# Kernel tuning notes

Measured on AMD Instinct MI355X. Metric: run time of the kernel, lower is better.

The kernel has to match this reference:

```python
import jax, jax.numpy as jnp
import numpy as np


def _ln(x, g, b, eps=1e-5):
    m = x.mean(-1, keepdims=True)
    v = ((x - m) ** 2).mean(-1, keepdims=True)
    return (x - m) * jax.lax.rsqrt(v + eps) * g + b


def setup_inputs() -> dict:
    key = jax.random.key(0)
    ks = jax.random.split(key, 16)
    B, C, D, H, W = 1, 192, 8, 32, 32
    nh, k, hid = 6, 7, 768
    n = lambda i, shape: jax.random.normal(ks[i], shape, dtype=jnp.float32) * 0.02
    return {
        'x': jax.random.normal(ks[0], (B, C, D, H, W), dtype=jnp.float32),
        'pos_emb': n(1, (1, D, C)),
        't_ln1_g': jnp.ones((C,), jnp.float32), 't_ln1_b': jnp.zeros((C,), jnp.float32),
        't_qkv_w': n(2, (C, 3 * C)),
        't_out_w': n(3, (C, C)), 't_out_b': jnp.zeros((C,), jnp.float32),
        't_ln2_g': jnp.ones((C,), jnp.float32), 't_ln2_b': jnp.zeros((C,), jnp.float32),
        't_fc1_w': n(4, (C, hid)), 't_fc1_b': jnp.zeros((hid,), jnp.float32),
        't_fc2_w': n(5, (hid, C)), 't_fc2_b': jnp.zeros((C,), jnp.float32),
        't_lnf_g': jnp.ones((C,), jnp.float32), 't_lnf_b': jnp.zeros((C,), jnp.float32),
        's_ln1_g': jnp.ones((C,), jnp.float32), 's_ln1_b': jnp.zeros((C,), jnp.float32),
        's_qkv_w': n(6, (C, 3 * C)), 's_qkv_b': jnp.zeros((3 * C,), jnp.float32),
        's_rpb': n(7, (nh, 2 * k - 1, 2 * k - 1)),
        's_proj_w': n(8, (C, C)), 's_proj_b': jnp.zeros((C,), jnp.float32),
        's_ln2_g': jnp.ones((C,), jnp.float32), 's_ln2_b': jnp.zeros((C,), jnp.float32),
        's_fc1_w': n(9, (C, hid)), 's_fc1_b': jnp.zeros((hid,), jnp.float32),
        's_fc2_w': n(10, (hid, C)), 's_fc2_b': jnp.zeros((C,), jnp.float32),
    }


def reference(x, pos_emb, t_ln1_g, t_ln1_b, t_qkv_w, t_out_w, t_out_b,
              t_ln2_g, t_ln2_b, t_fc1_w, t_fc1_b, t_fc2_w, t_fc2_b,
              t_lnf_g, t_lnf_b, s_ln1_g, s_ln1_b, s_qkv_w, s_qkv_b, s_rpb,
              s_proj_w, s_proj_b, s_ln2_g, s_ln2_b, s_fc1_w, s_fc1_b,
              s_fc2_w, s_fc2_b):
    B, C, D, H, W = x.shape
    nh = 6
    d = C // nh
    k = 7
    scale = d ** -0.5

    # ---- Time transformer: attend over the D frames per spatial position ----
    t = jnp.transpose(x, (0, 3, 4, 2, 1)).reshape(B * H * W, D, C)  # (b h w) s c
    t = t + pos_emb
    y = _ln(t, t_ln1_g, t_ln1_b)
    qkv = (y @ t_qkv_w).reshape(-1, D, 3, nh, d)
    q, kk, v = [jnp.transpose(qkv[:, :, i], (0, 2, 1, 3)) for i in range(3)]  # [N,nh,D,d]
    att = jax.nn.softmax(jnp.einsum('nhid,nhjd->nhij', q, kk) * scale, axis=-1)
    o = jnp.einsum('nhij,nhjd->nhid', att, v)
    o = jnp.transpose(o, (0, 2, 1, 3)).reshape(-1, D, C)
    t = t + (o @ t_out_w + t_out_b)
    y = _ln(t, t_ln2_g, t_ln2_b)
    t = t + (jax.nn.gelu(y @ t_fc1_w + t_fc1_b, approximate=False) @ t_fc2_w + t_fc2_b)
    t = _ln(t, t_lnf_g, t_lnf_b)
    x = x + jnp.transpose(t.reshape(B, H, W, D, C), (0, 4, 3, 1, 2))

    # ---- Space transformer: neighborhood (NAT) attention per frame ----
    s = jnp.transpose(x, (0, 2, 3, 4, 1)).reshape(B * D, H, W, C)  # (b s) h w c
    shortcut = s
    y = _ln(s, s_ln1_g, s_ln1_b)
    qkv = (y @ s_qkv_w + s_qkv_b).reshape(B * D, H, W, 3, nh, d)
    qkv = jnp.transpose(qkv, (3, 0, 4, 1, 2, 5))  # [3,N,nh,H,W,d]
    q, kk, v = qkv[0] * scale, qkv[1], qkv[2]
    half = k // 2
    sh = jnp.clip(jnp.arange(H) - half, 0, H - k)   # window start per row (edge-clamped)
    sw = jnp.clip(jnp.arange(W) - half, 0, W - k)
    idx_h = sh[:, None] + jnp.arange(k)             # [H,k] neighbor rows
    idx_w = sw[:, None] + jnp.arange(k)             # [W,k] neighbor cols
    rel_h = idx_h - jnp.arange(H)[:, None] + (k - 1)  # rel-pos-bias indices in [0,2k-2]
    rel_w = idx_w - jnp.arange(W)[:, None] + (k - 1)
    Kn = kk[:, :, idx_h][:, :, :, :, idx_w]  # [N,nh,H,k,W,k,d]
    Vn = v[:, :, idx_h][:, :, :, :, idx_w]
    att = jnp.einsum('nehwd,nehawbd->nehwab', q, Kn)  # [N,nh,H,W,k,k]
    bias = jnp.transpose(s_rpb[:, rel_h][:, :, :, rel_w], (0, 1, 3, 2, 4))  # [nh,H,W,k,k]
    att = att + bias[None]
    shp = att.shape
    att = jax.nn.softmax(att.reshape(shp[0], shp[1], shp[2], shp[3], k * k), axis=-1).reshape(shp)
    o = jnp.einsum('nehwab,nehawbd->nehwd', att, Vn)
    o = jnp.transpose(o, (0, 2, 3, 1, 4)).reshape(B * D, H, W, C)
    s = shortcut + (o @ s_proj_w + s_proj_b)
    y = _ln(s, s_ln2_g, s_ln2_b)
    s = s + (jax.nn.gelu(y @ s_fc1_w + s_fc1_b, approximate=False) @ s_fc2_w + s_fc2_b)
    x_space = jnp.transpose(s.reshape(B, D, H, W, C), (0, 4, 1, 2, 3))
    return x + x_space
```

## Files before the change

kernel.cpp:

```cpp
#include <hip/hip_runtime.h>
#include <hip/hip_bf16.h>
#include <math.h>

typedef __hip_bfloat16 bf16;
typedef short bf16x8 __attribute__((ext_vector_type(8)));
typedef float f32x4 __attribute__((ext_vector_type(4)));

__device__ __forceinline__ float b2f(bf16 v) { return __bfloat162float(v); }
__device__ __forceinline__ bf16 f2b(float v) { return __float2bfloat16(v); }
__device__ __forceinline__ float us2f(unsigned short u) {
  return __uint_as_float(((unsigned)u) << 16);
}
__device__ __forceinline__ unsigned short f2us(float f) {
  bf16 h = __float2bfloat16(f);
  return *reinterpret_cast<unsigned short*>(&h);
}
__device__ __forceinline__ float ldin(const void* p, size_t i, int f32) {
  return f32 ? ((const float*)p)[i] : b2f(((const bf16*)p)[i]);
}

#define CC 192
#define DD 8
#define HH 32
#define WW 32
#define NHEAD 6
#define HDIM 32
#define HID 768
#define NTOK 8192
#define ATT_SCALE 0.17677669529663687f

__global__ void probe_dtype_kernel(const unsigned short* __restrict__ xu,
                                   int* __restrict__ flag) {
  if (threadIdx.x == 0 && blockIdx.x == 0) {
    int insane = 0;
    for (int i = 0; i < 256; i++) {
      float v = us2f(xu[i]);
      float a = fabsf(v);
      bool sane = (a == 0.0f) || (a > 9.5e-7f && a < 64.0f);
      if (!sane) insane++;
    }
    *flag = (insane > 32) ? 1 : 0;
  }
}

__global__ void build_ln1_kernel(const void* __restrict__ x, const void* __restrict__ pos,
                                 const void* __restrict__ g, const void* __restrict__ b,
                                 float* __restrict__ T, bf16* __restrict__ Y,
                                 const int* __restrict__ dfl) {
  int f32 = *dfl;
  int wave = (blockIdx.x * blockDim.x + threadIdx.x) >> 6;
  int lane = threadIdx.x & 63;
  if (wave >= NTOK) return;
  int d = wave & 7, hw = wave >> 3;
  float v[3];
#pragma unroll
  for (int e = 0; e < 3; e++) {
    int c = lane + e * 64;
    v[e] = ldin(x, (size_t)((c << 3) + d) * 1024 + hw, f32) +
           ldin(pos, (size_t)d * CC + c, f32);
  }
  float* tr = T + (size_t)wave * CC;
#pragma unroll
  for (int e = 0; e < 3; e++) tr[lane + e * 64] = v[e];
  float s = v[0] + v[1] + v[2];
  for (int off = 32; off; off >>= 1) s += __shfl_xor(s, off);
  float mean = s * (1.0f / CC);
  float d0 = v[0] - mean, d1 = v[1] - mean, d2 = v[2] - mean;
  float q = d0 * d0 + d1 * d1 + d2 * d2;
  for (int off = 32; off; off >>= 1) q += __shfl_xor(q, off);
  float rstd = rsqrtf(q * (1.0f / CC) + 1e-5f);
  bf16* o = Y + (size_t)wave * CC;
  o[lane]       = f2b(d0 * rstd * ldin(g, lane, f32)       + ldin(b, lane, f32));
  o[lane + 64]  = f2b(d1 * rstd * ldin(g, lane + 64, f32)  + ldin(b, lane + 64, f32));
  o[lane + 128] = f2b(d2 * rstd * ldin(g, lane + 128, f32) + ldin(b, lane + 128, f32));
}

__global__ void ln_kernel(const float* __restrict__ in, bf16* __restrict__ out,
                          const void* __restrict__ g, const void* __restrict__ b,
                          int rows, const int* __restrict__ dfl) {
  int f32 = *dfl;
  int wave = (blockIdx.x * blockDim.x + threadIdx.x) >> 6;
  int lane = threadIdx.x & 63;
  if (wave >= rows) return;
  const float* r = in + (size_t)wave * CC;
  float v0 = r[lane], v1 = r[lane + 64], v2 = r[lane + 128];
  float s = v0 + v1 + v2;
  for (int off = 32; off; off >>= 1) s += __shfl_xor(s, off);
  float mean = s * (1.0f / CC);
  float d0 = v0 - mean, d1 = v1 - mean, d2 = v2 - mean;
  float q = d0 * d0 + d1 * d1 + d2 * d2;
  for (int off = 32; off; off >>= 1) q += __shfl_xor(q, off);
  float rstd = rsqrtf(q * (1.0f / CC) + 1e-5f);
  bf16* o = out + (size_t)wave * CC;
  o[lane]       = f2b(d0 * rstd * ldin(g, lane, f32)       + ldin(b, lane, f32));
  o[lane + 64]  = f2b(d1 * rstd * ldin(g, lane + 64, f32)  + ldin(b, lane + 64, f32));
  o[lane + 128] = f2b(d2 * rstd * ldin(g, lane + 128, f32) + ldin(b, lane + 128, f32));
}

template <int TM, bool BIAS, bool GELU, bool RES, bool OUTBF, bool FINAL>
__global__ void gemm_kernel(const bf16* __restrict__ A, const void* __restrict__ W,
                            const void* __restrict__ bias, const float* __restrict__ R,
                            void* __restrict__ Cout, const float* __restrict__ X2,
                            int M, int N, int K, const int* __restrict__ dfl) {
  int f32 = *dfl;
  __shared__ __align__(16) unsigned short As[TM * 64 * 40];
  __shared__ __align__(16) unsigned short Bs[64 * 40];
  int bm = blockIdx.y * (TM * 64), bn = blockIdx.x * 64;
  int tid = threadIdx.x;
  int w = tid >> 6;
  int lane = tid & 63;
  int lm = lane & 15;
  int lk = lane >> 4;

  f32x4 acc[TM][4];
#pragma unroll
  for (int i = 0; i < TM; i++)
#pragma unroll
    for (int j = 0; j < 4; j++) acc[i][j] = (f32x4){0.f, 0.f, 0.f, 0.f};

  const unsigned short* Au = reinterpret_cast<const unsigned short*>(A);

  for (int k0 = 0; k0 < K; k0 += 32) {
#pragma unroll
    for (int u = 0; u < TM; u++) {
      int unit = tid + u * 256;
      int row = unit >> 2, seg = unit & 3;
      uint4 v = *reinterpret_cast<const uint4*>(
          &Au[(size_t)(bm + row) * K + k0 + seg * 8]);
      *reinterpret_cast<uint4*>(&As[row * 40 + seg * 8]) = v;
    }
    {
      int e0 = tid * 8;
      int kk = e0 >> 6, n0 = e0 & 63;
      unsigned short vals[8];
      if (f32) {
        const float* Wf = (const float*)W + (size_t)(k0 + kk) * N + bn + n0;
        float4 w0 = *reinterpret_cast<const float4*>(Wf);
        float4 w1 = *reinterpret_cast<const float4*>(Wf + 4);
        vals[0] = f2us(w0.x); vals[1] = f2us(w0.y); vals[2] = f2us(w0.z); vals[3] = f2us(w0.w);
        vals[4] = f2us(w1.x); vals[5] = f2us(w1.y); vals[6] = f2us(w1.z); vals[7] = f2us(w1.w);
      } else {
        const unsigned short* Wb = (const unsigned short*)W + (size_t)(k0 + kk) * N + bn + n0;
        ushort4 u0 = *reinterpret_cast<const ushort4*>(Wb);
        ushort4 u1 = *reinterpret_cast<const ushort4*>(Wb + 4);
        vals[0] = u0.x; vals[1] = u0.y; vals[2] = u0.z; vals[3] = u0.w;
        vals[4] = u1.x; vals[5] = u1.y; vals[6] = u1.z; vals[7] = u1.w;
      }
#pragma unroll
      for (int j = 0; j < 8; j++) Bs[(n0 + j) * 40 + kk] = vals[j];
    }
    __syncthreads();

    bf16x8 af[TM], bfr[4];
#pragma unroll
    for (int tm = 0; tm < TM; tm++)
      af[tm] = *reinterpret_cast<const bf16x8*>(
          &As[(w * (TM * 16) + tm * 16 + lm) * 40 + lk * 8]);
#pragma unroll
    for (int tn = 0; tn < 4; tn++)
      bfr[tn] = *reinterpret_cast<const bf16x8*>(
          &Bs[(tn * 16 + lm) * 40 + lk * 8]);
#pragma unroll
    for (int tm = 0; tm < TM; tm++)
#pragma unroll
      for (int tn = 0; tn < 4; tn++)
        acc[tm][tn] = __builtin_amdgcn_mfma_f32_16x16x32_bf16(
            af[tm], bfr[tn], acc[tm][tn], 0, 0, 0);
    __syncthreads();
  }

#pragma unroll
  for (int tn = 0; tn < 4; tn++) {
    int col = bn + tn * 16 + lm;
    float bv = BIAS ? ldin(bias, col, f32) : 0.f;
#pragma unroll
    for (int tm = 0; tm < TM; tm++) {
      int row0 = bm + w * (TM * 16) + tm * 16 + lk * 4;
#pragma unroll
      for (int r = 0; r < 4; r++) {
        int row = row0 + r;
        float v = acc[tm][tn][r];
        if (BIAS) v += bv;
        if (GELU) v = 0.5f * v * (1.0f + erff(v * 0.70710678118654752f));
        size_t idx = (size_t)row * N + col;
        if (RES) v += R[idx];
        if (FINAL) {
          float o = v + X2[(size_t)row * CC + col];
          if (f32) ((float*)Cout)[(size_t)col * NTOK + row] = o;
          else     ((bf16*)Cout)[(size_t)col * NTOK + row] = f2b(o);
        } else if (OUTBF) {
          ((bf16*)Cout)[idx] = f2b(v);
        } else {
          ((float*)Cout)[idx] = v;
        }
      }
    }
  }
}

__global__ void time_attn_kernel(const bf16* __restrict__ qkv, bf16* __restrict__ O) {
  __shared__ float q[NHEAD][DD][HDIM];
  __shared__ float k[NHEAD][DD][HDIM];
  __shared__ float v[NHEAD][DD][HDIM];
  __shared__ float p[NHEAD][DD][DD];
  int n = blockIdx.x;
  int head = threadIdx.x >> 5;
  int dd = threadIdx.x & 31;
  for (int s = 0; s < DD; s++) {
    const bf16* row = qkv + (size_t)(n * DD + s) * (3 * CC);
    q[head][s][dd] = b2f(row[head * HDIM + dd]);
    k[head][s][dd] = b2f(row[CC + head * HDIM + dd]);
    v[head][s][dd] = b2f(row[2 * CC + head * HDIM + dd]);
  }
  __syncthreads();
  for (int pair = dd; pair < 64; pair += 32) {
    int sq = pair >> 3, sk = pair & 7;
    float sum = 0.f;
#pragma unroll
    for (int e = 0; e < HDIM; e++) sum += q[head][sq][e] * k[head][sk][e];
    p[head][sq][sk] = sum * ATT_SCALE;
  }
  __syncthreads();
  if (dd < DD) {
    float mx = -1e30f;
    for (int sk = 0; sk < DD; sk++) mx = fmaxf(mx, p[head][dd][sk]);
    float sum = 0.f;
    for (int sk = 0; sk < DD; sk++) { float e = expf(p[head][dd][sk] - mx); p[head][dd][sk] = e; sum += e; }
    float inv = 1.0f / sum;
    for (int sk = 0; sk < DD; sk++) p[head][dd][sk] *= inv;
  }
  __syncthreads();
  for (int sq = 0; sq < DD; sq++) {
    float sum = 0.f;
#pragma unroll
    for (int sk = 0; sk < DD; sk++) sum += p[head][sq][sk] * v[head][sk][dd];
    O[(size_t)(n * DD + sq) * CC + head * HDIM + dd] = f2b(sum);
  }
}

__global__ void epi_ln1_kernel(const float* __restrict__ T, const void* __restrict__ x,
                               const void* __restrict__ gf, const void* __restrict__ bf,
                               const void* __restrict__ g1, const void* __restrict__ b1,
                               float* __restrict__ X1T, bf16* __restrict__ Y,
                               const int* __restrict__ dfl) {
  int f32 = *dfl;
  int wave = (blockIdx.x * blockDim.x + threadIdx.x) >> 6;
  int lane = threadIdx.x & 63;
  if (wave >= NTOK) return;
  const float* r = T + (size_t)wave * CC;
  float v0 = r[lane], v1 = r[lane + 64], v2 = r[lane + 128];
  float s = v0 + v1 + v2;
  for (int off = 32; off; off >>= 1) s += __shfl_xor(s, off);
  float mean = s * (1.0f / CC);
  float d0 = v0 - mean, d1 = v1 - mean, d2 = v2 - mean;
  float q = d0 * d0 + d1 * d1 + d2 * d2;
  for (int off = 32; off; off >>= 1) q += __shfl_xor(q, off);
  float rstd = rsqrtf(q * (1.0f / CC) + 1e-5f);
  int d = wave & 7, hw = wave >> 3;
  int m = d * 1024 + hw;
  float xv[3];
#pragma unroll
  for (int e = 0; e < 3; e++) {
    int c = lane + e * 64;
    float dv = (e == 0 ? d0 : (e == 1 ? d1 : d2));
    float normed = dv * rstd * ldin(gf, c, f32) + ldin(bf, c, f32);
    xv[e] = ldin(x, (size_t)((c << 3) + d) * 1024 + hw, f32) + normed;
  }
  float* o = X1T + (size_t)m * CC;
#pragma unroll
  for (int e = 0; e < 3; e++) o[lane + e * 64] = xv[e];
  float s2 = xv[0] + xv[1] + xv[2];
  for (int off = 32; off; off >>= 1) s2 += __shfl_xor(s2, off);
  float mean2 = s2 * (1.0f / CC);
  float e0 = xv[0] - mean2, e1 = xv[1] - mean2, e2 = xv[2] - mean2;
  float q2 = e0 * e0 + e1 * e1 + e2 * e2;
  for (int off = 32; off; off >>= 1) q2 += __shfl_xor(q2, off);
  float rstd2 = rsqrtf(q2 * (1.0f / CC) + 1e-5f);
  bf16* y = Y + (size_t)m * CC;
  y[lane]       = f2b(e0 * rstd2 * ldin(g1, lane, f32)       + ldin(b1, lane, f32));
  y[lane + 64]  = f2b(e1 * rstd2 * ldin(g1, lane + 64, f32)  + ldin(b1, lane + 64, f32));
  y[lane + 128] = f2b(e2 * rstd2 * ldin(g1, lane + 128, f32) + ldin(b1, lane + 128, f32));
}

#define NKEY 224
#define PKS 40
#define PVS 232
__global__ void nat_attn_kernel(const bf16* __restrict__ qkv, const void* __restrict__ rpb,
                                bf16* __restrict__ O, const int* __restrict__ dfl) {
  int f32 = *dfl;
  __shared__ __align__(16) unsigned short Ks[NKEY * PKS];
  __shared__ __align__(16) unsigned short Vs[32 * PVS];
  __shared__ __align__(16) unsigned short Qs[64 * PKS];
  __shared__ __align__(16) unsigned short Ps[64 * PVS];
  __shared__ float rb[176];

  int blk = blockIdx.x;
  int frame = blk & 7;
  int rest = blk >> 3;
  int h = rest % 6;
  int tile = rest / 6;
  int ty = tile >> 2, tx = tile & 3;
  int base_h = min(max(ty * 8 - 3, 0), HH - 7);
  int base_w = min(max(tx * 8 - 3, 0), WW - 7);

  int tid = threadIdx.x;

  for (int i = tid; i < 169; i += 256) rb[i] = ldin(rpb, (size_t)h * 169 + i, f32);
  for (int u = tid; u < 784; u += 256) {
    int j = u >> 2, seg = u & 3;
    int a = j / 14, bb = j - a * 14;
    int ih = min(base_h + a, HH - 1), iw = min(base_w + bb, WW - 1);
    int mg = frame * 1024 + ih * 32 + iw;
    uint4 v = *reinterpret_cast<const uint4*>(qkv + (size_t)mg * 576 + 192 + h * 32 + seg * 8);
    *reinterpret_cast<uint4*>(&Ks[j * PKS + seg * 8]) = v;
  }
  for (int u = tid; u < 784; u += 256) {
    int j = u >> 2, seg = u & 3;
    int a = j / 14, bb = j - a * 14;
    int ih = min(base_h + a, HH - 1), iw = min(base_w + bb, WW - 1);
    int mg = frame * 1024 + ih * 32 + iw;
    uint4 v = *reinterpret_cast<const uint4*>(qkv + (size_t)mg * 576 + 384 + h * 32 + seg * 8);
    unsigned arr[4] = {v.x, v.y, v.z, v.w};
#pragma unroll
    for (int e = 0; e < 4; e++) {
      Vs[(seg * 8 + e * 2) * PVS + j]     = (unsigned short)(arr[e] & 0xffffu);
      Vs[(seg * 8 + e * 2 + 1) * PVS + j] = (unsigned short)(arr[e] >> 16);
    }
  }
  for (int u = tid; u < 32 * (PVS - 196); u += 256) {
    int dd = u / (PVS - 196), c = 196 + u % (PVS - 196);
    Vs[dd * PVS + c] = 0;
  }
  {
    int q = tid >> 2, seg = tid & 3;
    int qy = ty * 8 + (q >> 3), qx = tx * 8 + (q & 7);
    int mg = frame * 1024 + qy * 32 + qx;
    uint4 v = *reinterpret_cast<const uint4*>(qkv + (size_t)mg * 576 + h * 32 + seg * 8);
    *reinterpret_cast<uint4*>(&Qs[q * PKS + seg * 8]) = v;
  }
  __syncthreads();

  int w = tid >> 6;
  int lane = tid & 63;
  int c = lane & 15;
  int lk = lane >> 4;

  bf16x8 aq = *reinterpret_cast<const bf16x8*>(&Qs[(w * 16 + c) * PKS + lk * 8]);
  f32x4 sc[14];
#pragma unroll
  for (int f = 0; f < 14; f++) {
    bf16x8 bk = *reinterpret_cast<const bf16x8*>(&Ks[(f * 16 + c) * PKS + lk * 8]);
    sc[f] = __builtin_amdgcn_mfma_f32_16x16x32_bf16(aq, bk, (f32x4){0.f, 0.f, 0.f, 0.f}, 0, 0, 0);
  }

#pragma unroll
  for (int f = 0; f < 14; f++) {
    int key = f * 16 + c;
    int a = key / 14, bb = key - a * 14;
    int ih = base_h + a, iw = base_w + bb;
    bool keyok = key < 196;
#pragma unroll
    for (int r = 0; r < 4; r++) {
      int qloc = w * 16 + lk * 4 + r;
      int qy = ty * 8 + (qloc >> 3), qx = tx * 8 + (qloc & 7);
      int sh = min(max(qy - 3, 0), HH - 7);
      int sw = min(max(qx - 3, 0), WW - 7);
      bool valid = keyok && ((unsigned)(ih - sh) < 7u) && ((unsigned)(iw - sw) < 7u);
      int bidx = valid ? (ih - qy + 6) * 13 + (iw - qx + 6) : 0;
      float s = sc[f][r] * ATT_SCALE + rb[bidx];
      sc[f][r] = valid ? s : -1e30f;
    }
  }

  float mx[4], sm[4];
#pragma unroll
  for (int r = 0; r < 4; r++) {
    float m = sc[0][r];
#pragma unroll
    for (int f = 1; f < 14; f++) m = fmaxf(m, sc[f][r]);
    for (int off = 8; off; off >>= 1) m = fmaxf(m, __shfl_xor(m, off));
    mx[r] = m;
    float s = 0.f;
#pragma unroll
    for (int f = 0; f < 14; f++) { float e = __expf(sc[f][r] - m); sc[f][r] = e; s += e; }
    for (int off = 8; off; off >>= 1) s += __shfl_xor(s, off);
    sm[r] = 1.0f / s;
  }
#pragma unroll
  for (int f = 0; f < 14; f++)
#pragma unroll
    for (int r = 0; r < 4; r++)
      Ps[(w * 16 + lk * 4 + r) * PVS + f * 16 + c] = f2us(sc[f][r] * sm[r]);
  __syncthreads();

  f32x4 oacc[2] = {(f32x4){0.f, 0.f, 0.f, 0.f}, (f32x4){0.f, 0.f, 0.f, 0.f}};
#pragma unroll
  for (int kt = 0; kt < 7; kt++) {
    bf16x8 ap = *reinterpret_cast<const bf16x8*>(&Ps[(w * 16 + c) * PVS + kt * 32 + lk * 8]);
#pragma unroll
    for (int dt = 0; dt < 2; dt++) {
      bf16x8 bv = *reinterpret_cast<const bf16x8*>(&Vs[(dt * 16 + c) * PVS + kt * 32 + lk * 8]);
      oacc[dt] = __builtin_amdgcn_mfma_f32_16x16x32_bf16(ap, bv, oacc[dt], 0, 0, 0);
    }
  }

#pragma unroll
  for (int dt = 0; dt < 2; dt++)
#pragma unroll
    for (int r = 0; r < 4; r++) {
      int qloc = w * 16 + lk * 4 + r;
      int qy = ty * 8 + (qloc >> 3), qx = tx * 8 + (qloc & 7);
      int mg = frame * 1024 + qy * 32 + qx;
      O[(size_t)mg * CC + h * 32 + dt * 16 + c] = f2b(oacc[dt][r]);
    }
}

extern "C" void kernel_launch(void* const* d_in, const int* in_sizes, int n_in,
                              void* d_out, int out_size, void* d_ws, size_t ws_size,
                              hipStream_t stream) {
  const void* x        = d_in[0];
  const void* pos_emb  = d_in[1];
  const void* t_ln1_g  = d_in[2];
  const void* t_ln1_b  = d_in[3];
  const void* t_qkv_w  = d_in[4];
  const void* t_out_w  = d_in[5];
  const void* t_out_b  = d_in[6];
  const void* t_ln2_g  = d_in[7];
  const void* t_ln2_b  = d_in[8];
  const void* t_fc1_w  = d_in[9];
  const void* t_fc1_b  = d_in[10];
  const void* t_fc2_w  = d_in[11];
  const void* t_fc2_b  = d_in[12];
  const void* t_lnf_g  = d_in[13];
  const void* t_lnf_b  = d_in[14];
  const void* s_ln1_g  = d_in[15];
  const void* s_ln1_b  = d_in[16];
  const void* s_qkv_w  = d_in[17];
  const void* s_qkv_b  = d_in[18];
  const void* s_rpb    = d_in[19];
  const void* s_proj_w = d_in[20];
  const void* s_proj_b = d_in[21];
  const void* s_ln2_g  = d_in[22];
  const void* s_ln2_b  = d_in[23];
  const void* s_fc1_w  = d_in[24];
  const void* s_fc1_b  = d_in[25];
  const void* s_fc2_w  = d_in[26];
  const void* s_fc2_b  = d_in[27];

  float* ws = (float*)d_ws;
  const size_t SZ = (size_t)NTOK * CC;
  const size_t need = (5 * SZ + 4) * sizeof(float);
  if (ws_size < need) return;

  float* T   = ws;
  float* X1T = ws + SZ;
  bf16*  Y   = (bf16*)(ws + 2 * SZ);
  bf16*  O   = (bf16*)(ws + 2 * SZ + SZ / 2);
  bf16*  QKV = (bf16*)(ws + 3 * SZ);
  bf16*  Hb  = QKV;
  float* S   = T;
  int*   dfl = (int*)(ws + 5 * SZ);

  dim3 blk256(256);

  probe_dtype_kernel<<<1, 64, 0, stream>>>((const unsigned short*)x, dfl);

  build_ln1_kernel<<<NTOK / 4, blk256, 0, stream>>>(x, pos_emb, t_ln1_g, t_ln1_b, T, Y, dfl);
  gemm_kernel<2, false, false, false, true, false><<<dim3(9, 64), blk256, 0, stream>>>(
      Y, t_qkv_w, nullptr, nullptr, QKV, nullptr, NTOK, 3 * CC, CC, dfl);
  time_attn_kernel<<<1024, 192, 0, stream>>>(QKV, O);
  gemm_kernel<1, true, false, true, false, false><<<dim3(3, 128), blk256, 0, stream>>>(
      O, t_out_w, t_out_b, T, T, nullptr, NTOK, CC, CC, dfl);
  ln_kernel<<<NTOK / 4, blk256, 0, stream>>>(T, Y, t_ln2_g, t_ln2_b, NTOK, dfl);
  gemm_kernel<2, true, true, false, true, false><<<dim3(12, 64), blk256, 0, stream>>>(
      Y, t_fc1_w, t_fc1_b, nullptr, Hb, nullptr, NTOK, HID, CC, dfl);
  gemm_kernel<1, true, false, true, false, false><<<dim3(3, 128), blk256, 0, stream>>>(
      Hb, t_fc2_w, t_fc2_b, T, T, nullptr, NTOK, CC, HID, dfl);
  epi_ln1_kernel<<<NTOK / 4, blk256, 0, stream>>>(
      T, x, t_lnf_g, t_lnf_b, s_ln1_g, s_ln1_b, X1T, Y, dfl);

  gemm_kernel<2, true, false, false, true, false><<<dim3(9, 64), blk256, 0, stream>>>(
      Y, s_qkv_w, s_qkv_b, nullptr, QKV, nullptr, NTOK, 3 * CC, CC, dfl);
  nat_attn_kernel<<<768, blk256, 0, stream>>>(QKV, s_rpb, O, dfl);
  gemm_kernel<1, true, false, true, false, false><<<dim3(3, 128), blk256, 0, stream>>>(
      O, s_proj_w, s_proj_b, X1T, S, nullptr, NTOK, CC, CC, dfl);
  ln_kernel<<<NTOK / 4, blk256, 0, stream>>>(S, Y, s_ln2_g, s_ln2_b, NTOK, dfl);
  gemm_kernel<2, true, true, false, true, false><<<dim3(12, 64), blk256, 0, stream>>>(
      Y, s_fc1_w, s_fc1_b, nullptr, Hb, nullptr, NTOK, HID, CC, dfl);
  gemm_kernel<1, true, false, true, false, true><<<dim3(3, 128), blk256, 0, stream>>>(
      Hb, s_fc2_w, s_fc2_b, S, d_out, X1T, NTOK, CC, HID, dfl);
}
```

Measured before the change: 304.6 us.

## Pre-transpose weights to bf16 and widen GEMM K-tile to 64

Adds a kernel that converts all eight weight matrices once per call into transposed bf16 [N,K] layout in workspace. The GEMM then loads B tiles with 16-byte vector copies instead of per-element scattered shared-memory stores and fp32-to-bf16 conversion. The K tile is doubled to 64 with padded LDS rows, halving the number of barriers per GEMM. It also parallelizes the dtype probe across a wave. The cost is one extra launch that moves about 5 MB of weights, plus more shared memory per block.

```diff
diff --git a/kernel.cpp b/kernel.cpp
--- a/kernel.cpp
+++ b/kernel.cpp
@@ -31,17 +31,45 @@
 
 __global__ void probe_dtype_kernel(const unsigned short* __restrict__ xu,
                                    int* __restrict__ flag) {
-  if (threadIdx.x == 0 && blockIdx.x == 0) {
-    int insane = 0;
-    for (int i = 0; i < 256; i++) {
-      float v = us2f(xu[i]);
-      float a = fabsf(v);
-      bool sane = (a == 0.0f) || (a > 9.5e-7f && a < 64.0f);
-      if (!sane) insane++;
-    }
-    *flag = (insane > 32) ? 1 : 0;
-  }
-}
+  int lane = threadIdx.x;
+  int insane = 0;
+  for (int i = lane; i < 256; i += 64) {
+    float a = fabsf(us2f(xu[i]));
+    bool sane = (a == 0.0f) || (a > 9.5e-7f && a < 64.0f);
+    if (!sane) insane++;
+  }
+  for (int off = 32; off; off >>= 1) insane += __shfl_xor(insane, off);
+  if (lane == 0) *flag = (insane > 32) ? 1 : 0;
+}
+
+__global__ void wconv_kernel(const void* w0, const void* w1, const void* w2,
+                             const void* w3, const void* w4, const void* w5,
+                             const void* w6, const void* w7,
+                             bf16* __restrict__ WT, const int* __restrict__ dfl) {
+  int f32 = *dfl;
+  int idx = blockIdx.x * 256 + threadIdx.x;
+  if (idx >= 884736) return;
+  const void* src; int K, N, loc;
+  if      (idx < 110592) { src = w0; K = 192; N = 576; loc = idx; }
+  else if (idx < 147456) { src = w1; K = 192; N = 192; loc = idx - 110592; }
+  else if (idx < 294912) { src = w2; K = 192; N = 768; loc = idx - 147456; }
+  else if (idx < 442368) { src = w3; K = 768; N = 192; loc = idx - 294912; }
+  else if (idx < 552960) { src = w4; K = 192; N = 576; loc = idx - 442368; }
+  else if (idx < 589824) { src = w5; K = 192; N = 192; loc = idx - 552960; }
+  else if (idx < 737280) { src = w6; K = 192; N = 768; loc = idx - 589824; }
+  else                   { src = w7; K = 768; N = 192; loc = idx - 737280; }
+  int n = loc / K, k = loc - n * K;
+  WT[idx] = f2b(ldin(src, (size_t)k * N + n, f32));
+}
+
+#define WOFF_TQKV  0
+#define WOFF_TOUT  110592
+#define WOFF_TFC1  147456
+#define WOFF_TFC2  294912
+#define WOFF_SQKV  442368
+#define WOFF_SPROJ 552960
+#define WOFF_SFC1  589824
+#define WOFF_SFC2  737280
 
 __global__ void build_ln1_kernel(const void* __restrict__ x, const void* __restrict__ pos,
                                  const void* __restrict__ g, const void* __restrict__ b,
@@ -98,13 +126,13 @@
 }
 
 template <int TM, bool BIAS, bool GELU, bool RES, bool OUTBF, bool FINAL>
-__global__ void gemm_kernel(const bf16* __restrict__ A, const void* __restrict__ W,
+__global__ void gemm_kernel(const bf16* __restrict__ A, const bf16* __restrict__ WT,
                             const void* __restrict__ bias, const float* __restrict__ R,
                             void* __restrict__ Cout, const float* __restrict__ X2,
                             int M, int N, int K, const int* __restrict__ dfl) {
   int f32 = *dfl;
-  __shared__ __align__(16) unsigned short As[TM * 64 * 40];
-  __shared__ __align__(16) unsigned short Bs[64 * 40];
+  __shared__ __align__(16) unsigned short As[TM * 64 * 72];
+  __shared__ __align__(16) unsigned short Bs[64 * 72];
   int bm = blockIdx.y * (TM * 64), bn = blockIdx.x * 64;
   int tid = threadIdx.x;
   int w = tid >> 6;
@@ -119,53 +147,45 @@
     for (int j = 0; j < 4; j++) acc[i][j] = (f32x4){0.f, 0.f, 0.f, 0.f};
 
   const unsigned short* Au = reinterpret_cast<const unsigned short*>(A);
-
-  for (int k0 = 0; k0 < K; k0 += 32) {
-#pragma unroll
-    for (int u = 0; u < TM; u++) {
+  const unsigned short* Wu = reinterpret_cast<const unsigned short*>(WT);
+
+  for (int k0 = 0; k0 < K; k0 += 64) {
+#pragma unroll
+    for (int u = 0; u < TM * 2; u++) {
       int unit = tid + u * 256;
-      int row = unit >> 2, seg = unit & 3;
+      int row = unit >> 3, seg = unit & 7;
       uint4 v = *reinterpret_cast<const uint4*>(
           &Au[(size_t)(bm + row) * K + k0 + seg * 8]);
-      *reinterpret_cast<uint4*>(&As[row * 40 + seg * 8]) = v;
-    }
-    {
-      int e0 = tid * 8;
-      int kk = e0 >> 6, n0 = e0 & 63;
-      unsigned short vals[8];
-      if (f32) {
-        const float* Wf = (const float*)W + (size_t)(k0 + kk) * N + bn + n0;
-        float4 w0 = *reinterpret_cast<const float4*>(Wf);
-        float4 w1 = *reinterpret_cast<const float4*>(Wf + 4);
-        vals[0] = f2us(w0.x); vals[1] = f2us(w0.y); vals[2] = f2us(w0.z); vals[3] = f2us(w0.w);
-        vals[4] = f2us(w1.x); vals[5] = f2us(w1.y); vals[6] = f2us(w1.z); vals[7] = f2us(w1.w);
-      } else {
-        const unsigned short* Wb = (const unsigned short*)W + (size_t)(k0 + kk) * N + bn + n0;
-        ushort4 u0 = *reinterpret_cast<const ushort4*>(Wb);
-        ushort4 u1 = *reinterpret_cast<const ushort4*>(Wb + 4);
-        vals[0] = u0.x; vals[1] = u0.y; vals[2] = u0.z; vals[3] = u0.w;
-        vals[4] = u1.x; vals[5] = u1.y; vals[6] = u1.z; vals[7] = u1.w;
-      }
-#pragma unroll
-      for (int j = 0; j < 8; j++) Bs[(n0 + j) * 40 + kk] = vals[j];
+      *reinterpret_cast<uint4*>(&As[row * 72 + seg * 8]) = v;
+    }
+#pragma unroll
+    for (int u = 0; u < 2; u++) {
+      int unit = tid + u * 256;
+      int n = unit >> 3, seg = unit & 7;
+      uint4 v = *reinterpret_cast<const uint4*>(
+          &Wu[(size_t)(bn + n) * K + k0 + seg * 8]);
+      *reinterpret_cast<uint4*>(&Bs[n * 72 + seg * 8]) = v;
     }
     __syncthreads();
 
-    bf16x8 af[TM], bfr[4];
-#pragma unroll
-    for (int tm = 0; tm < TM; tm++)
-      af[tm] = *reinterpret_cast<const bf16x8*>(
-          &As[(w * (TM * 16) + tm * 16 + lm) * 40 + lk * 8]);
-#pragma unroll
-    for (int tn = 0; tn < 4; tn++)
-      bfr[tn] = *reinterpret_cast<const bf16x8*>(
-          &Bs[(tn * 16 + lm) * 40 + lk * 8]);
-#pragma unroll
-    for (int tm = 0; tm < TM; tm++)
+#pragma unroll
+    for (int kc = 0; kc < 2; kc++) {
+      bf16x8 af[TM], bfr[4];
+#pragma unroll
+      for (int tm = 0; tm < TM; tm++)
+        af[tm] = *reinterpret_cast<const bf16x8*>(
+            &As[(w * (TM * 16) + tm * 16 + lm) * 72 + kc * 32 + lk * 8]);
 #pragma unroll
       for (int tn = 0; tn < 4; tn++)
-        acc[tm][tn] = __builtin_amdgcn_mfma_f32_16x16x32_bf16(
-            af[tm], bfr[tn], acc[tm][tn], 0, 0, 0);
+        bfr[tn] = *reinterpret_cast<const bf16x8*>(
+            &Bs[(tn * 16 + lm) * 72 + kc * 32 + lk * 8]);
+#pragma unroll
+      for (int tm = 0; tm < TM; tm++)
+#pragma unroll
+        for (int tn = 0; tn < 4; tn++)
+          acc[tm][tn] = __builtin_amdgcn_mfma_f32_16x16x32_bf16(
+              af[tm], bfr[tn], acc[tm][tn], 0, 0, 0);
+    }
     __syncthreads();
   }
 
@@ -372,14 +392,13 @@
     }
   }
 
-  float mx[4], sm[4];
+  float sm[4];
 #pragma unroll
   for (int r = 0; r < 4; r++) {
     float m = sc[0][r];
 #pragma unroll
     for (int f = 1; f < 14; f++) m = fmaxf(m, sc[f][r]);
     for (int off = 8; off; off >>= 1) m = fmaxf(m, __shfl_xor(m, off));
-    mx[r] = m;
     float s = 0.f;
 #pragma unroll
     for (int f = 0; f < 14; f++) { float e = __expf(sc[f][r] - m); sc[f][r] = e; s += e; }
@@ -449,7 +468,7 @@
 
   float* ws = (float*)d_ws;
   const size_t SZ = (size_t)NTOK * CC;
-  const size_t need = (5 * SZ + 4) * sizeof(float);
+  const size_t need = (5 * SZ + 4 + 442368 + 16) * sizeof(float);
   if (ws_size < need) return;
 
   float* T   = ws;
@@ -460,33 +479,36 @@
   bf16*  Hb  = QKV;
   float* S   = T;
   int*   dfl = (int*)(ws + 5 * SZ);
+  bf16*  WT  = (bf16*)(ws + 5 * SZ + 4);
 
   dim3 blk256(256);
 
   probe_dtype_kernel<<<1, 64, 0, stream>>>((const unsigned short*)x, dfl);
+  wconv_kernel<<<3456, blk256, 0, stream>>>(
+      t_qkv_w, t_out_w, t_fc1_w, t_fc2_w, s_qkv_w, s_proj_w, s_fc1_w, s_fc2_w, WT, dfl);
 
   build_ln1_kernel<<<NTOK / 4, blk256, 0, stream>>>(x, pos_emb, t_ln1_g, t_ln1_b, T, Y, dfl);
   gemm_kernel<2, false, false, false, true, false><<<dim3(9, 64), blk256, 0, stream>>>(
-      Y, t_qkv_w, nullptr, nullptr, QKV, nullptr, NTOK, 3 * CC, CC, dfl);
+      Y, WT + WOFF_TQKV, nullptr, nullptr, QKV, nullptr, NTOK, 3 * CC, CC, dfl);
   time_attn_kernel<<<1024, 192, 0, stream>>>(QKV, O);
   gemm_kernel<1, true, false, true, false, false><<<dim3(3, 128), blk256, 0, stream>>>(
-      O, t_out_w, t_out_b, T, T, nullptr, NTOK, CC, CC, dfl);
+      O, WT + WOFF_TOUT, t_out_b, T, T, nullptr, NTOK, CC, CC, dfl);
   ln_kernel<<<NTOK / 4, blk256, 0, stream>>>(T, Y, t_ln2_g, t_ln2_b, NTOK, dfl);
   gemm_kernel<2, true, true, false, true, false><<<dim3(12, 64), blk256, 0, stream>>>(
-      Y, t_fc1_w, t_fc1_b, nullptr, Hb, nullptr, NTOK, HID, CC, dfl);
+      Y, WT + WOFF_TFC1, t_fc1_b, nullptr, Hb, nullptr, NTOK, HID, CC, dfl);
   gemm_kernel<1, true, false, true, false, false><<<dim3(3, 128), blk256, 0, stream>>>(
-      Hb, t_fc2_w, t_fc2_b, T, T, nullptr, NTOK, CC, HID, dfl);
+      Hb, WT + WOFF_TFC2, t_fc2_b, T, T, nullptr, NTOK, CC, HID, dfl);
   epi_ln1_kernel<<<NTOK / 4, blk256, 0, stream>>>(
       T, x, t_lnf_g, t_lnf_b, s_ln1_g, s_ln1_b, X1T, Y, dfl);
 
   gemm_kernel<2, true, false, false, true, false><<<dim3(9, 64), blk256, 0, stream>>>(
-      Y, s_qkv_w, s_qkv_b, nullptr, QKV, nullptr, NTOK, 3 * CC, CC, dfl);
+      Y, WT + WOFF_SQKV, s_qkv_b, nullptr, QKV, nullptr, NTOK, 3 * CC, CC, dfl);
   nat_attn_kernel<<<768, blk256, 0, stream>>>(QKV, s_rpb, O, dfl);
   gemm_kernel<1, true, false, true, false, false><<<dim3(3, 128), blk256, 0, stream>>>(
-      O, s_proj_w, s_proj_b, X1T, S, nullptr, NTOK, CC, CC, dfl);
+      O, WT + WOFF_SPROJ, s_proj_b, X1T, S, nullptr, NTOK, CC, CC, dfl);
   ln_kernel<<<NTOK / 4, blk256, 0, stream>>>(S, Y, s_ln2_g, s_ln2_b, NTOK, dfl);
   gemm_kernel<2, true, true, false, true, false><<<dim3(12, 64), blk256, 0, stream>>>(
-      Y, s_fc1_w, s_fc1_b, nullptr, Hb, nullptr, NTOK, HID, CC, dfl);
+      Y, WT + WOFF_SFC1, s_fc1_b, nullptr, Hb, nullptr, NTOK, HID, CC, dfl);
   gemm_kernel<1, true, false, true, false, true><<<dim3(3, 128), blk256, 0, stream>>>(
-      Hb, s_fc2_w, s_fc2_b, S, d_out, X1T, NTOK, CC, HID, dfl);
-}
+      Hb, WT + WOFF_SFC2, s_fc2_b, S, d_out, X1T, NTOK, CC, HID, dfl);
+}
```

New measurement: 279.7 us. -8.2%, faster.
